# Performance work log

Measured on AMD Instinct MI355X. Metric: run time of the kernel, lower is better.

## Reference

```python
import jax, jax.numpy as jnp
import numpy as np

KNOW, ITEM, D, L, LAT, B, S = 1024, 20000, 128, 2, 256, 256, 200
NTOT = ITEM + KNOW
E1, E2 = 32768, 160000


def graph_layer(h, W, a, src, dst, n):
    # GAT-style: gather src/dst, edge MLP, segment softmax over dst, weighted scatter-sum
    z = h @ W                                              # [N, D]
    e = jax.nn.leaky_relu((jnp.concatenate([z[src], z[dst]], axis=-1) @ a)[:, 0])  # [E]
    m = jax.ops.segment_max(e, dst, num_segments=n)
    m = jnp.where(jnp.isfinite(m), m, 0.0)                 # nodes with no in-edges
    w = jnp.exp(e - m[dst])                                # [E]
    den = jax.ops.segment_sum(w, dst, num_segments=n)      # [N]
    num = jax.ops.segment_sum(w[:, None] * z[src], dst, num_segments=n)  # [N, D]
    return jnp.where(den[:, None] > 0, num / jnp.maximum(den, 1e-12)[:, None], 0.0)


def setup_inputs() -> dict:
    key = jax.random.key(0)
    ks = jax.random.split(key, 32)
    p = lambda i, shp: jax.random.normal(ks[i], shp, dtype=jnp.float32) * 0.05
    inp = {
        'p_rec': jax.random.randint(ks[0], (B, S), 0, ITEM),
        'p_target': jax.random.randint(ks[1], (B,), 0, S),
        'a_rec': jax.random.randint(ks[2], (B, S), 0, 3),
        'kn_rec': jax.random.uniform(ks[3], (B, S, KNOW), dtype=jnp.float32),
        'kn_num': jnp.ones((B, S), dtype=jnp.float32),
        'src1': jax.random.randint(ks[4], (E1,), 0, KNOW),
        'dst1': jax.random.randint(ks[5], (E1,), 0, KNOW),
        'src2': jax.random.randint(ks[6], (E2,), 0, NTOT),
        'dst2': jax.random.randint(ks[7], (E2,), 0, NTOT),
        'src3': jax.random.randint(ks[8], (E2,), 0, NTOT),
        'dst3': jax.random.randint(ks[9], (E2,), 0, NTOT),
        'kn_table': p(10, (KNOW, D)),
        'exer_table': p(11, (ITEM, D)),
        'ans_table': p(12, (3, D)),
        'gW': p(13, (L, 3, D, D)),
        'gA': p(14, (L, 3, 2 * D, 1)),
        'raW1': p(15, (L, D, D)),
        'raB1': jnp.zeros((L, D), jnp.float32),
        'raW2': p(16, (L, D, 1)),
        'actW1': p(17, (3 * D, LAT)),
        'actB1': jnp.zeros((LAT,), jnp.float32),
        'actW2': p(18, (LAT, ITEM)),
        'actB2': jnp.zeros((ITEM,), jnp.float32),
        'vW1': p(19, (3, 3 * D, LAT)),
        'vB1': jnp.zeros((3, LAT), jnp.float32),
        'vW2': p(20, (3, LAT, 1)),
        'vB2': jnp.zeros((3, 1), jnp.float32),
    }
    return inp


def reference(p_rec, p_target, a_rec, kn_rec, kn_num, src1, dst1, src2, dst2, src3, dst3,
              kn_table, exer_table, ans_table, gW, gA, raW1, raB1, raW2,
              actW1, actB1, actW2, actB2, vW1, vB1, vW2, vB2):
    kn, ex = kn_table, exer_table
    for l in range(L):  # GraphEncoder: stacked Fusion blocks (distinct params)
        k_dir = graph_layer(kn, gW[l, 0], gA[l, 0], src1, dst1, KNOW)
        ek = jnp.concatenate([ex, kn], axis=0)             # [NTOT, D]
        kfe = graph_layer(ek, gW[l, 1], gA[l, 1], src2, dst2, NTOT)
        efk = graph_layer(ek, gW[l, 2], gA[l, 2], src3, dst3, NTOT)
        A_, B_ = k_dir, kfe[ITEM:]
        ra = lambda x: jnp.tanh(x @ raW1[l] + raB1[l]) @ raW2[l]  # [KNOW, 1]
        s = jax.nn.softmax(jnp.concatenate([ra(A_), ra(B_)], axis=1), axis=1)
        kn = s[:, :1] * A_ + s[:, 1:2] * B_
        ex = efk[:ITEM]
    # hidden_layer
    be = ex[p_rec]                                         # [B, S, D]
    ba = ans_table[a_rec]                                  # [B, S, D]
    bk = jnp.einsum('bsk,kd->bsd', kn_rec, kn) / kn_num[..., None]
    item = jnp.concatenate([be, ba, bk], axis=-1)          # [B, S, 3D]
    m = (jnp.arange(S)[None, :] < (p_target + 1)[:, None]).astype(item.dtype)
    h = (item * m[..., None]).sum(axis=1) / m.sum(axis=1, keepdims=True)  # [B, 3D]
    logits = jnp.tanh(h @ actW1 + actB1) @ actW2 + actB2   # [B, ITEM]
    vh = jnp.tanh(jnp.einsum('bd,kdl->kbl', h, vW1) + vB1[:, None, :])
    vals = jnp.einsum('kbl,klo->kbo', vh, vW2) + vB2[:, None, :]  # [3, B, 1]
    return logits, vals[0], vals[1], vals[2]
```

## Files before the change

kernel.cpp:

```cpp
#include <hip/hip_runtime.h>

#define D 128
#define KNOW 1024
#define ITEM 20000
#define NTOT (ITEM + KNOW)
#define LAYERS 2
#define LAT 256
#define BB 256
#define SS 200
#define H3 (3 * D)
#define CH 8
#define ZROWS 64
#define NBK (KNOW / ZROWS)
#define NBN ((NTOT + ZROWS - 1) / ZROWS)
#define XPITCH 68

__global__ __launch_bounds__(256) void zdv(
    const float* __restrict__ Xe, const float* __restrict__ Xk,
    const float* __restrict__ gW, const float* __restrict__ gA, int layer,
    float* __restrict__ z1, float* __restrict__ z2, float* __restrict__ z3,
    float* __restrict__ ds1, float* __restrict__ dd1,
    float* __restrict__ ds2, float* __restrict__ dd2,
    float* __restrict__ ds3, float* __restrict__ dd3)
{
    __shared__ __align__(16) float xT[D * XPITCH];
    int bid = blockIdx.x;
    int g, row0, nmax;
    if (bid < NBK)            { g = 0; row0 = bid * ZROWS;                nmax = KNOW; }
    else if (bid < NBK + NBN) { g = 1; row0 = (bid - NBK) * ZROWS;        nmax = NTOT; }
    else                      { g = 2; row0 = (bid - NBK - NBN) * ZROWS;  nmax = NTOT; }
    const float* W = gW + (size_t)(layer * 3 + g) * D * D;
    const float* A = gA + (size_t)(layer * 3 + g) * 2 * D;
    float* Z  = (g == 0) ? z1  : (g == 1 ? z2  : z3);
    float* DS = (g == 0) ? ds1 : (g == 1 ? ds2 : ds3);
    float* DD = (g == 0) ? dd1 : (g == 1 ? dd2 : dd3);

    int tid = threadIdx.x;
#pragma unroll
    for (int i = 0; i < 8; ++i) {
        int flat = tid + i * 256;
        int row  = flat >> 5;
        int f4   = flat & 31;
        int grow = row0 + row;
        float4 v = make_float4(0.f, 0.f, 0.f, 0.f);
        if (grow < nmax) {
            const float* src = (g == 0) ? (Xk + (size_t)grow * D)
                             : (grow < ITEM ? Xe + (size_t)grow * D
                                            : Xk + (size_t)(grow - ITEM) * D);
            v = *(const float4*)(src + f4 * 4);
        }
        int slot = row ^ ((f4 & 7) << 2);
        int kk = f4 * 4;
        xT[(kk + 0) * XPITCH + slot] = v.x;
        xT[(kk + 1) * XPITCH + slot] = v.y;
        xT[(kk + 2) * XPITCH + slot] = v.z;
        xT[(kk + 3) * XPITCH + slot] = v.w;
    }
    __syncthreads();

    int cg = tid & 31;
    int rg = tid >> 5;
    int c0 = cg * 4;
    int r0a = rg * 8, r0b = rg * 8 + 4;

    float acc[8][4];
#pragma unroll
    for (int r = 0; r < 8; ++r)
#pragma unroll
        for (int c = 0; c < 4; ++c) acc[r][c] = 0.f;

#pragma unroll 4
    for (int k = 0; k < D; ++k) {
        float4 wv = *(const float4*)(W + (size_t)k * D + c0);
        int xc = ((k >> 2) & 7) << 2;
        float4 xa = *(const float4*)&xT[k * XPITCH + (r0a ^ xc)];
        float4 xb = *(const float4*)&xT[k * XPITCH + (r0b ^ xc)];
        acc[0][0] = fmaf(xa.x, wv.x, acc[0][0]); acc[0][1] = fmaf(xa.x, wv.y, acc[0][1]);
        acc[0][2] = fmaf(xa.x, wv.z, acc[0][2]); acc[0][3] = fmaf(xa.x, wv.w, acc[0][3]);
        acc[1][0] = fmaf(xa.y, wv.x, acc[1][0]); acc[1][1] = fmaf(xa.y, wv.y, acc[1][1]);
        acc[1][2] = fmaf(xa.y, wv.z, acc[1][2]); acc[1][3] = fmaf(xa.y, wv.w, acc[1][3]);
        acc[2][0] = fmaf(xa.z, wv.x, acc[2][0]); acc[2][1] = fmaf(xa.z, wv.y, acc[2][1]);
        acc[2][2] = fmaf(xa.z, wv.z, acc[2][2]); acc[2][3] = fmaf(xa.z, wv.w, acc[2][3]);
        acc[3][0] = fmaf(xa.w, wv.x, acc[3][0]); acc[3][1] = fmaf(xa.w, wv.y, acc[3][1]);
        acc[3][2] = fmaf(xa.w, wv.z, acc[3][2]); acc[3][3] = fmaf(xa.w, wv.w, acc[3][3]);
        acc[4][0] = fmaf(xb.x, wv.x, acc[4][0]); acc[4][1] = fmaf(xb.x, wv.y, acc[4][1]);
        acc[4][2] = fmaf(xb.x, wv.z, acc[4][2]); acc[4][3] = fmaf(xb.x, wv.w, acc[4][3]);
        acc[5][0] = fmaf(xb.y, wv.x, acc[5][0]); acc[5][1] = fmaf(xb.y, wv.y, acc[5][1]);
        acc[5][2] = fmaf(xb.y, wv.z, acc[5][2]); acc[5][3] = fmaf(xb.y, wv.w, acc[5][3]);
        acc[6][0] = fmaf(xb.z, wv.x, acc[6][0]); acc[6][1] = fmaf(xb.z, wv.y, acc[6][1]);
        acc[6][2] = fmaf(xb.z, wv.z, acc[6][2]); acc[6][3] = fmaf(xb.z, wv.w, acc[6][3]);
        acc[7][0] = fmaf(xb.w, wv.x, acc[7][0]); acc[7][1] = fmaf(xb.w, wv.y, acc[7][1]);
        acc[7][2] = fmaf(xb.w, wv.z, acc[7][2]); acc[7][3] = fmaf(xb.w, wv.w, acc[7][3]);
    }

#pragma unroll
    for (int r = 0; r < 8; ++r) {
        int grow = row0 + ((r < 4) ? (r0a + r) : (r0b + r - 4));
        if (grow < nmax) {
            float4 v = make_float4(acc[r][0], acc[r][1], acc[r][2], acc[r][3]);
            *(float4*)(Z + (size_t)grow * D + c0) = v;
        }
    }

    float4 as = *(const float4*)(A + c0);
    float4 ad = *(const float4*)(A + D + c0);
    float ps[8], pd[8];
#pragma unroll
    for (int r = 0; r < 8; ++r) {
        ps[r] = acc[r][0] * as.x + acc[r][1] * as.y + acc[r][2] * as.z + acc[r][3] * as.w;
        pd[r] = acc[r][0] * ad.x + acc[r][1] * ad.y + acc[r][2] * ad.z + acc[r][3] * ad.w;
    }
#pragma unroll
    for (int m = 16; m; m >>= 1) {
#pragma unroll
        for (int r = 0; r < 8; ++r) {
            ps[r] += __shfl_xor(ps[r], m, 64);
            pd[r] += __shfl_xor(pd[r], m, 64);
        }
    }
    if (cg == 0) {
#pragma unroll
        for (int r = 0; r < 8; ++r) {
            int grow = row0 + ((r < 4) ? (r0a + r) : (r0b + r - 4));
            if (grow < nmax) { DS[grow] = ps[r]; DD[grow] = pd[r]; }
        }
    }
}

__global__ void hist3(const int* __restrict__ d1, const int* __restrict__ d2, const int* __restrict__ d3,
                      int E1, int E2, int* __restrict__ c1, int* __restrict__ c2, int* __restrict__ c3) {
    int i = blockIdx.x * blockDim.x + threadIdx.x;
    if (i < E1) atomicAdd(&c1[d1[i]], 1);
    else if (i < E1 + E2) { int d = d2[i - E1]; if (d >= ITEM) atomicAdd(&c2[d - ITEM], 1); }
    else if (i < E1 + 2 * E2) { int d = d3[i - E1 - E2]; if (d < ITEM) atomicAdd(&c3[d], 1); }
}

__global__ __launch_bounds__(1024) void exscan3(int* __restrict__ c1, int* __restrict__ o1,
                                                int* __restrict__ c2, int* __restrict__ o2,
                                                int* __restrict__ c3, int* __restrict__ o3) {
    int g = blockIdx.x;
    int* cnt = (g == 0) ? c1 : (g == 1 ? c2 : c3);
    int* off = (g == 0) ? o1 : (g == 1 ? o2 : o3);
    int n = (g == 2) ? ITEM : KNOW;
    int tid = threadIdx.x, lane = tid & 63, wid = tid >> 6;
    int L = (n + 1023) >> 10;
    int i0 = tid * L;
    int sum = 0;
    for (int q = 0; q < L; ++q) {
        int i = i0 + q;
        if (i < n) sum += cnt[i];
    }
    int x = sum;
#pragma unroll
    for (int d = 1; d < 64; d <<= 1) { int t = __shfl_up(x, d, 64); if (lane >= d) x += t; }
    __shared__ int ws[16];
    if (lane == 63) ws[wid] = x;
    __syncthreads();
    if (wid == 0) {
        int w = (lane < 16) ? ws[lane] : 0;
#pragma unroll
        for (int d = 1; d < 16; d <<= 1) { int t = __shfl_up(w, d, 64); if (lane >= d) w += t; }
        if (lane < 16) ws[lane] = w;
    }
    __syncthreads();
    int run = x - sum + ((wid > 0) ? ws[wid - 1] : 0);
    if (tid == 0) off[0] = 0;
    for (int q = 0; q < L; ++q) {
        int i = i0 + q;
        if (i < n) {
            int v = cnt[i];
            cnt[i] = run;
            run += v;
            off[i + 1] = run;
        }
    }
}

__global__ void scatter3(const int* __restrict__ s1, const int* __restrict__ d1,
                         const int* __restrict__ s2, const int* __restrict__ d2,
                         const int* __restrict__ s3, const int* __restrict__ d3,
                         int E1, int E2, int* __restrict__ cur1, int* __restrict__ cur2, int* __restrict__ cur3,
                         int* __restrict__ e1, int* __restrict__ e2, int* __restrict__ e3) {
    int i = blockIdx.x * blockDim.x + threadIdx.x;
    if (i < E1) { int p = atomicAdd(&cur1[d1[i]], 1); e1[p] = s1[i]; }
    else if (i < E1 + E2) { int j = i - E1; int d = d2[j]; if (d >= ITEM) { int p = atomicAdd(&cur2[d - ITEM], 1); e2[p] = s2[j]; } }
    else if (i < E1 + 2 * E2) { int j = i - E1 - E2; int d = d3[j]; if (d < ITEM) { int p = atomicAdd(&cur3[d], 1); e3[p] = s3[j]; } }
}

__device__ __forceinline__ void agg_row(const float* __restrict__ Z, const float* __restrict__ dsrc,
                                        float dd, const int* __restrict__ es, int e0, int e1,
                                        int lane, float* __restrict__ acc) {
#pragma unroll
    for (int q = 0; q < 8; ++q) acc[q] = 0.f;
    if (e1 <= e0) return;
    float mx = -3.4e38f;
    for (int e = e0 + lane; e < e1; e += 64) {
        float t = dsrc[es[e]] + dd;
        t = (t > 0.f) ? t : 0.01f * t;
        mx = fmaxf(mx, t);
    }
#pragma unroll
    for (int o = 32; o; o >>= 1) mx = fmaxf(mx, __shfl_xor(mx, o, 64));
    int eg = lane >> 4, cs = lane & 15;
    float den = 0.f;
    for (int e = e0 + eg; e < e1; e += 4) {
        int s = es[e];
        float t = dsrc[s] + dd;
        t = (t > 0.f) ? t : 0.01f * t;
        float w = __expf(t - mx);
        den += w;
        const float4* zr = (const float4*)(Z + (size_t)s * D + cs * 8);
        float4 za = zr[0], zb = zr[1];
        acc[0] = fmaf(w, za.x, acc[0]); acc[1] = fmaf(w, za.y, acc[1]);
        acc[2] = fmaf(w, za.z, acc[2]); acc[3] = fmaf(w, za.w, acc[3]);
        acc[4] = fmaf(w, zb.x, acc[4]); acc[5] = fmaf(w, zb.y, acc[5]);
        acc[6] = fmaf(w, zb.z, acc[6]); acc[7] = fmaf(w, zb.w, acc[7]);
    }
#pragma unroll
    for (int m = 16; m <= 32; m <<= 1) {
        den += __shfl_xor(den, m, 64);
#pragma unroll
        for (int q = 0; q < 8; ++q) acc[q] += __shfl_xor(acc[q], m, 64);
    }
    float inv = 1.f / fmaxf(den, 1e-12f);
#pragma unroll
    for (int q = 0; q < 8; ++q) acc[q] *= inv;
}

__global__ __launch_bounds__(256) void agg3c(
    const float* __restrict__ z1, const float* __restrict__ z2, const float* __restrict__ z3,
    const float* __restrict__ ds1, const float* __restrict__ dd1,
    const float* __restrict__ ds2, const float* __restrict__ dd2,
    const float* __restrict__ ds3, const float* __restrict__ dd3,
    const int* __restrict__ off1, const int* __restrict__ es1,
    const int* __restrict__ off2, const int* __restrict__ es2,
    const int* __restrict__ off3, const int* __restrict__ es3,
    const float* __restrict__ raW1, const float* __restrict__ raB1,
    const float* __restrict__ raW2, float* __restrict__ buf)
{
    int wv = threadIdx.x >> 6, lane = threadIdx.x & 63;
    int eg = lane >> 4, cs = lane & 15;
    if (blockIdx.x < KNOW / 4) {
        __shared__ float ABs[4][2][D];
        int i = blockIdx.x * 4 + wv;
        float accA[8], accB[8];
        agg_row(z1, ds1, dd1[i], es1, off1[i], off1[i + 1], lane, accA);
        agg_row(z2, ds2, dd2[ITEM + i], es2, off2[i], off2[i + 1], lane, accB);
        if (eg == 0) {
            *(float4*)&ABs[wv][0][cs * 8]     = make_float4(accA[0], accA[1], accA[2], accA[3]);
            *(float4*)&ABs[wv][0][cs * 8 + 4] = make_float4(accA[4], accA[5], accA[6], accA[7]);
            *(float4*)&ABs[wv][1][cs * 8]     = make_float4(accB[0], accB[1], accB[2], accB[3]);
            *(float4*)&ABs[wv][1][cs * 8 + 4] = make_float4(accB[4], accB[5], accB[6], accB[7]);
        }
        __syncthreads();
        int j0 = lane * 2;
        float b0 = raB1[j0], b1 = raB1[j0 + 1];
        float aA0 = b0, aA1 = b1, aB0 = b0, aB1 = b1;
#pragma unroll 4
        for (int k = 0; k < D; ++k) {
            float av = ABs[wv][0][k], bv = ABs[wv][1][k];
            float2 w = *(const float2*)(raW1 + (size_t)k * D + j0);
            aA0 = fmaf(av, w.x, aA0); aA1 = fmaf(av, w.y, aA1);
            aB0 = fmaf(bv, w.x, aB0); aB1 = fmaf(bv, w.y, aB1);
        }
        float2 w2 = *(const float2*)(raW2 + j0);
        float pA = tanhf(aA0) * w2.x + tanhf(aA1) * w2.y;
        float pB = tanhf(aB0) * w2.x + tanhf(aB1) * w2.y;
#pragma unroll
        for (int o = 32; o; o >>= 1) { pA += __shfl_xor(pA, o, 64); pB += __shfl_xor(pB, o, 64); }
        float mx2 = fmaxf(pA, pB);
        float eA = __expf(pA - mx2), eB = __expf(pB - mx2);
        float s = 1.f / (eA + eB);
        float sA = eA * s, sB = eB * s;
        float2 Av = *(float2*)&ABs[wv][0][j0];
        float2 Bv = *(float2*)&ABs[wv][1][j0];
        *(float2*)(buf + (size_t)(ITEM + i) * D + j0) =
            make_float2(sA * Av.x + sB * Bv.x, sA * Av.y + sB * Bv.y);
    } else {
        int row = (blockIdx.x - KNOW / 4) * 4 + wv;
        if (row < ITEM) {
            float acc[8];
            agg_row(z3, ds3, dd3[row], es3, off3[row], off3[row + 1], lane, acc);
            if (eg == 0) {
                *(float4*)(buf + (size_t)row * D + cs * 8)     = make_float4(acc[0], acc[1], acc[2], acc[3]);
                *(float4*)(buf + (size_t)row * D + cs * 8 + 4) = make_float4(acc[4], acc[5], acc[6], acc[7]);
            }
        }
    }
}

__global__ __launch_bounds__(256) void krowk(const float* __restrict__ kn_rec, const float* __restrict__ kn_num,
                                             const int* __restrict__ p_target, float* __restrict__ krowP) {
    int b = blockIdx.x, ch = blockIdx.y;
    int cnt = p_target[b] + 1;
    int per = (SS + CH - 1) / CH;
    int s0 = ch * per, s1 = s0 + per;
    if (s1 > cnt) s1 = cnt;
    int k0 = threadIdx.x * 4;
    float4 a = make_float4(0.f, 0.f, 0.f, 0.f);
    for (int s = s0; s < s1; ++s) {
        float inv = 1.f / kn_num[b * SS + s];
        float4 v = *(const float4*)(kn_rec + ((size_t)b * SS + s) * KNOW + k0);
        a.x += v.x * inv; a.y += v.y * inv; a.z += v.z * inv; a.w += v.w * inv;
    }
    *(float4*)(krowP + ((size_t)ch * BB + b) * KNOW + k0) = a;
}

__global__ __launch_bounds__(512) void hker(const float* __restrict__ ex, const float* __restrict__ ans_table,
                                            const int* __restrict__ p_rec, const int* __restrict__ a_rec,
                                            const int* __restrict__ p_target, const float* __restrict__ krowP,
                                            const float* __restrict__ kn, float* __restrict__ h) {
    int b = blockIdx.x;
    int j = threadIdx.x & 127, sg = threadIdx.x >> 7;
    int cnt = p_target[b] + 1;
    __shared__ int pidx[SS], aidx[SS];
    __shared__ float kr[KNOW];
    __shared__ float red[4][3][128];
    for (int i = threadIdx.x; i < cnt; i += 512) { pidx[i] = p_rec[b * SS + i]; aidx[i] = a_rec[b * SS + i]; }
    for (int i = threadIdx.x; i < KNOW; i += 512) {
        float s = 0.f;
#pragma unroll
        for (int c = 0; c < CH; ++c) s += krowP[((size_t)c * BB + b) * KNOW + i];
        kr[i] = s;
    }
    __syncthreads();
    float accE = 0.f, accA = 0.f;
    for (int s = sg; s < cnt; s += 4) {
        accE += ex[(size_t)pidx[s] * D + j];
        accA += ans_table[aidx[s] * D + j];
    }
    float accK = 0.f;
    for (int k = sg * 256; k < sg * 256 + 256; ++k) accK += kr[k] * kn[(size_t)k * D + j];
    red[sg][0][j] = accE; red[sg][1][j] = accA; red[sg][2][j] = accK;
    __syncthreads();
    if (sg == 0) {
        float inv = 1.f / (float)cnt;
        float e = (red[0][0][j] + red[1][0][j] + red[2][0][j] + red[3][0][j]) * inv;
        float a = (red[0][1][j] + red[1][1][j] + red[2][1][j] + red[3][1][j]) * inv;
        float kv = (red[0][2][j] + red[1][2][j] + red[2][2][j] + red[3][2][j]) * inv;
        h[b * H3 + j] = e;
        h[b * H3 + D + j] = a;
        h[b * H3 + 2 * D + j] = kv;
    }
}

__global__ __launch_bounds__(256) void hidden_gemm(const float* __restrict__ h,
                                                   const float* __restrict__ actW1, const float* __restrict__ actB1,
                                                   const float* __restrict__ vW1, const float* __restrict__ vB1,
                                                   float* __restrict__ hid) {
    __shared__ float hT[H3 * 17];
    int tid = threadIdx.x;
    int b0 = blockIdx.y * 16;
    for (int idx = tid; idx < 16 * H3; idx += 256) {
        int r = idx / H3, k = idx - r * H3;
        hT[k * 17 + r] = h[(size_t)(b0 + r) * H3 + k];
    }
    __syncthreads();
    int j = blockIdx.x * 64 + (tid & 63);
    int head = j >> 8, jj = j & 255;
    int rg = tid >> 6, r0 = rg * 4;
    const float* W = (head == 0) ? actW1 : (vW1 + (size_t)(head - 1) * H3 * LAT);
    float bias = (head == 0) ? actB1[jj] : vB1[(head - 1) * LAT + jj];
    float acc[4] = {bias, bias, bias, bias};
#pragma unroll 4
    for (int k = 0; k < H3; ++k) {
        float w = W[(size_t)k * LAT + jj];
        float h0 = hT[k * 17 + r0 + 0];
        float h1 = hT[k * 17 + r0 + 1];
        float h2 = hT[k * 17 + r0 + 2];
        float h3 = hT[k * 17 + r0 + 3];
        acc[0] = fmaf(h0, w, acc[0]);
        acc[1] = fmaf(h1, w, acc[1]);
        acc[2] = fmaf(h2, w, acc[2]);
        acc[3] = fmaf(h3, w, acc[3]);
    }
#pragma unroll
    for (int r = 0; r < 4; ++r)
        hid[((size_t)head * BB + (b0 + r0 + r)) * LAT + jj] = tanhf(acc[r]);
}

__global__ __launch_bounds__(256) void logitsker(const float* __restrict__ hid, const float* __restrict__ actW2,
                                                 const float* __restrict__ actB2, float* __restrict__ out) {
    __shared__ float hT[LAT * 33];
    int tid = threadIdx.x;
    int b0 = blockIdx.y * 32;
    for (int idx = tid; idx < 32 * LAT; idx += 256) {
        int r = idx >> 8, k = idx & 255;
        hT[k * 33 + r] = hid[(size_t)(b0 + r) * LAT + k];
    }
    __syncthreads();
    int lane6 = tid & 63;
    int rg = tid >> 6, r0 = rg * 8;
    int ibase = blockIdx.x * 256 + lane6;
    int icol[4], icl[4];
    float bias[4];
#pragma unroll
    for (int c = 0; c < 4; ++c) {
        icol[c] = ibase + c * 64;
        icl[c] = icol[c] < ITEM ? icol[c] : (ITEM - 1);
        bias[c] = actB2[icl[c]];
    }
    float acc[8][4];
#pragma unroll
    for (int r = 0; r < 8; ++r)
#pragma unroll
        for (int c = 0; c < 4; ++c) acc[r][c] = bias[c];
#pragma unroll 2
    for (int k = 0; k < LAT; ++k) {
        float w0 = actW2[(size_t)k * ITEM + icl[0]];
        float w1 = actW2[(size_t)k * ITEM + icl[1]];
        float w2 = actW2[(size_t)k * ITEM + icl[2]];
        float w3 = actW2[(size_t)k * ITEM + icl[3]];
        const float* hp = &hT[k * 33 + r0];
#pragma unroll
        for (int r = 0; r < 8; ++r) {
            float hv = hp[r];
            acc[r][0] = fmaf(hv, w0, acc[r][0]);
            acc[r][1] = fmaf(hv, w1, acc[r][1]);
            acc[r][2] = fmaf(hv, w2, acc[r][2]);
            acc[r][3] = fmaf(hv, w3, acc[r][3]);
        }
    }
#pragma unroll
    for (int c = 0; c < 4; ++c) {
        if (icol[c] < ITEM) {
#pragma unroll
            for (int r = 0; r < 8; ++r)
                out[(size_t)(b0 + r0 + r) * ITEM + icol[c]] = acc[r][c];
        }
    }
}

__global__ __launch_bounds__(256) void valsker(const float* __restrict__ hid, const float* __restrict__ vW2,
                                               const float* __restrict__ vB2, float* __restrict__ out) {
    int idx = blockIdx.x * 4 + (threadIdx.x >> 6);
    int lane = threadIdx.x & 63;
    if (idx >= 3 * BB) return;
    int k = idx / BB, b = idx - k * BB;
    const float* vh = hid + ((size_t)(k + 1) * BB + b) * LAT;
    float4 a = ((const float4*)vh)[lane];
    float4 w = ((const float4*)(vW2 + k * LAT))[lane];
    float s = a.x * w.x + a.y * w.y + a.z * w.z + a.w * w.w;
#pragma unroll
    for (int o = 32; o; o >>= 1) s += __shfl_down(s, o, 64);
    if (lane == 0) out[(size_t)BB * ITEM + k * BB + b] = s + vB2[k];
}

extern "C" void kernel_launch(void* const* d_in, const int* in_sizes, int n_in,
                              void* d_out, int out_size, void* d_ws, size_t ws_size,
                              hipStream_t stream) {
    const int*   p_rec      = (const int*)d_in[0];
    const int*   p_target   = (const int*)d_in[1];
    const int*   a_rec      = (const int*)d_in[2];
    const float* kn_rec     = (const float*)d_in[3];
    const float* kn_num     = (const float*)d_in[4];
    const int*   src1       = (const int*)d_in[5];
    const int*   dst1       = (const int*)d_in[6];
    const int*   src2       = (const int*)d_in[7];
    const int*   dst2       = (const int*)d_in[8];
    const int*   src3       = (const int*)d_in[9];
    const int*   dst3       = (const int*)d_in[10];
    const float* kn_table   = (const float*)d_in[11];
    const float* exer_table = (const float*)d_in[12];
    const float* ans_table  = (const float*)d_in[13];
    const float* gW         = (const float*)d_in[14];
    const float* gA         = (const float*)d_in[15];
    const float* raW1       = (const float*)d_in[16];
    const float* raB1       = (const float*)d_in[17];
    const float* raW2       = (const float*)d_in[18];
    const float* actW1      = (const float*)d_in[19];
    const float* actB1      = (const float*)d_in[20];
    const float* actW2      = (const float*)d_in[21];
    const float* actB2      = (const float*)d_in[22];
    const float* vW1        = (const float*)d_in[23];
    const float* vB1        = (const float*)d_in[24];
    const float* vW2        = (const float*)d_in[25];
    const float* vB2        = (const float*)d_in[26];
    const int E1 = in_sizes[5], E2 = in_sizes[7];

    float* base = (float*)d_ws;
    size_t o = 0;
    auto alloc = [&](size_t n) -> float* { float* p = base + o; o += (n + 3) & ~(size_t)3; return p; };
    float* buf  = alloc((size_t)NTOT * D);
    float* z1   = alloc((size_t)KNOW * D);
    float* z2   = alloc((size_t)NTOT * D);
    float* z3   = alloc((size_t)NTOT * D);
    float* ds1 = alloc(KNOW);  float* dd1 = alloc(KNOW);
    float* ds2 = alloc(NTOT);  float* dd2 = alloc(NTOT);
    float* ds3 = alloc(NTOT);  float* dd3 = alloc(NTOT);
    int* cnts = (int*)alloc(2 * KNOW + NTOT);
    int* cnt1 = cnts, *cnt2 = cnts + KNOW, *cnt3 = cnts + 2 * KNOW;
    int* off1 = (int*)alloc(KNOW + 1);
    int* off2 = (int*)alloc(KNOW + 1);
    int* off3 = (int*)alloc(ITEM + 1);
    int* es1  = (int*)alloc(E1);
    int* es2  = (int*)alloc(E2);
    int* es3  = (int*)alloc(E2);
    float* krowP = alloc((size_t)CH * BB * KNOW);
    float* hbuf  = alloc((size_t)BB * H3);
    float* hid   = alloc((size_t)4 * BB * LAT);

    hipMemsetAsync(cnts, 0, sizeof(int) * (2 * KNOW + NTOT), stream);

    int etot = E1 + 2 * E2;
    hist3<<<(etot + 255) / 256, 256, 0, stream>>>(dst1, dst2, dst3, E1, E2, cnt1, cnt2, cnt3);
    exscan3<<<3, 1024, 0, stream>>>(cnt1, off1, cnt2, off2, cnt3, off3);
    scatter3<<<(etot + 255) / 256, 256, 0, stream>>>(src1, dst1, src2, dst2, src3, dst3,
                                                     E1, E2, cnt1, cnt2, cnt3, es1, es2, es3);

    int aggBlocks = KNOW / 4 + ITEM / 4;
    for (int l = 0; l < LAYERS; ++l) {
        const float* Xe = (l == 0) ? exer_table : buf;
        const float* Xk = (l == 0) ? kn_table : (buf + (size_t)ITEM * D);
        zdv<<<NBK + 2 * NBN, 256, 0, stream>>>(Xe, Xk, gW, gA, l, z1, z2, z3,
                                               ds1, dd1, ds2, dd2, ds3, dd3);
        agg3c<<<aggBlocks, 256, 0, stream>>>(z1, z2, z3, ds1, dd1, ds2, dd2, ds3, dd3,
                                             off1, es1, off2, es2, off3, es3,
                                             raW1 + (size_t)l * D * D, raB1 + (size_t)l * D,
                                             raW2 + (size_t)l * D, buf);
    }

    krowk<<<dim3(BB, CH), 256, 0, stream>>>(kn_rec, kn_num, p_target, krowP);
    hker<<<BB, 512, 0, stream>>>(buf, ans_table, p_rec, a_rec, p_target, krowP, buf + (size_t)ITEM * D, hbuf);
    hidden_gemm<<<dim3(16, 16), 256, 0, stream>>>(hbuf, actW1, actB1, vW1, vB1, hid);
    logitsker<<<dim3((ITEM + 255) / 256, 8), 256, 0, stream>>>(hid, actW2, actB2, (float*)d_out);
    valsker<<<(3 * BB + 3) / 4, 256, 0, stream>>>(hid, vW2, vB2, (float*)d_out);
}
```

Before: 312.7 us.

## Fuse graph layers and krow reduction into a persistent cooperative kernel

```diff
diff --git a/kernel.cpp b/kernel.cpp
--- a/kernel.cpp
+++ b/kernel.cpp
@@ -1,4 +1,7 @@
 #include <hip/hip_runtime.h>
+#include <hip/hip_cooperative_groups.h>
+
+namespace cg = cooperative_groups;
 
 #define D 128
 #define KNOW 1024
@@ -13,18 +16,20 @@
 #define ZROWS 64
 #define NBK (KNOW / ZROWS)
 #define NBN ((NTOT + ZROWS - 1) / ZROWS)
+#define NZT (NBK + 2 * NBN)
+#define NAGGU (KNOW / 4 + ITEM / 4)
+#define NKROW (BB * CH)
 #define XPITCH 68
-
-__global__ __launch_bounds__(256) void zdv(
+#define MGRID 256
+
+__device__ __forceinline__ void zdv_tile(int bid, int layer, float* __restrict__ xT,
     const float* __restrict__ Xe, const float* __restrict__ Xk,
-    const float* __restrict__ gW, const float* __restrict__ gA, int layer,
+    const float* __restrict__ gW, const float* __restrict__ gA,
     float* __restrict__ z1, float* __restrict__ z2, float* __restrict__ z3,
     float* __restrict__ ds1, float* __restrict__ dd1,
     float* __restrict__ ds2, float* __restrict__ dd2,
     float* __restrict__ ds3, float* __restrict__ dd3)
 {
-    __shared__ __align__(16) float xT[D * XPITCH];
-    int bid = blockIdx.x;
     int g, row0, nmax;
     if (bid < NBK)            { g = 0; row0 = bid * ZROWS;                nmax = KNOW; }
     else if (bid < NBK + NBN) { g = 1; row0 = (bid - NBK) * ZROWS;        nmax = NTOT; }
@@ -36,6 +41,7 @@
     float* DD = (g == 0) ? dd1 : (g == 1 ? dd2 : dd3);
 
     int tid = threadIdx.x;
+    __syncthreads();
 #pragma unroll
     for (int i = 0; i < 8; ++i) {
         int flat = tid + i * 256;
@@ -58,9 +64,9 @@
     }
     __syncthreads();
 
-    int cg = tid & 31;
+    int cg_ = tid & 31;
     int rg = tid >> 5;
-    int c0 = cg * 4;
+    int c0 = cg_ * 4;
     int r0a = rg * 8, r0b = rg * 8 + 4;
 
     float acc[8][4];
@@ -118,73 +124,13 @@
             pd[r] += __shfl_xor(pd[r], m, 64);
         }
     }
-    if (cg == 0) {
+    if (cg_ == 0) {
 #pragma unroll
         for (int r = 0; r < 8; ++r) {
             int grow = row0 + ((r < 4) ? (r0a + r) : (r0b + r - 4));
             if (grow < nmax) { DS[grow] = ps[r]; DD[grow] = pd[r]; }
         }
     }
-}
-
-__global__ void hist3(const int* __restrict__ d1, const int* __restrict__ d2, const int* __restrict__ d3,
-                      int E1, int E2, int* __restrict__ c1, int* __restrict__ c2, int* __restrict__ c3) {
-    int i = blockIdx.x * blockDim.x + threadIdx.x;
-    if (i < E1) atomicAdd(&c1[d1[i]], 1);
-    else if (i < E1 + E2) { int d = d2[i - E1]; if (d >= ITEM) atomicAdd(&c2[d - ITEM], 1); }
-    else if (i < E1 + 2 * E2) { int d = d3[i - E1 - E2]; if (d < ITEM) atomicAdd(&c3[d], 1); }
-}
-
-__global__ __launch_bounds__(1024) void exscan3(int* __restrict__ c1, int* __restrict__ o1,
-                                                int* __restrict__ c2, int* __restrict__ o2,
-                                                int* __restrict__ c3, int* __restrict__ o3) {
-    int g = blockIdx.x;
-    int* cnt = (g == 0) ? c1 : (g == 1 ? c2 : c3);
-    int* off = (g == 0) ? o1 : (g == 1 ? o2 : o3);
-    int n = (g == 2) ? ITEM : KNOW;
-    int tid = threadIdx.x, lane = tid & 63, wid = tid >> 6;
-    int L = (n + 1023) >> 10;
-    int i0 = tid * L;
-    int sum = 0;
-    for (int q = 0; q < L; ++q) {
-        int i = i0 + q;
-        if (i < n) sum += cnt[i];
-    }
-    int x = sum;
-#pragma unroll
-    for (int d = 1; d < 64; d <<= 1) { int t = __shfl_up(x, d, 64); if (lane >= d) x += t; }
-    __shared__ int ws[16];
-    if (lane == 63) ws[wid] = x;
-    __syncthreads();
-    if (wid == 0) {
-        int w = (lane < 16) ? ws[lane] : 0;
-#pragma unroll
-        for (int d = 1; d < 16; d <<= 1) { int t = __shfl_up(w, d, 64); if (lane >= d) w += t; }
-        if (lane < 16) ws[lane] = w;
-    }
-    __syncthreads();
-    int run = x - sum + ((wid > 0) ? ws[wid - 1] : 0);
-    if (tid == 0) off[0] = 0;
-    for (int q = 0; q < L; ++q) {
-        int i = i0 + q;
-        if (i < n) {
-            int v = cnt[i];
-            cnt[i] = run;
-            run += v;
-            off[i + 1] = run;
-        }
-    }
-}
-
-__global__ void scatter3(const int* __restrict__ s1, const int* __restrict__ d1,
-                         const int* __restrict__ s2, const int* __restrict__ d2,
-                         const int* __restrict__ s3, const int* __restrict__ d3,
-                         int E1, int E2, int* __restrict__ cur1, int* __restrict__ cur2, int* __restrict__ cur3,
-                         int* __restrict__ e1, int* __restrict__ e2, int* __restrict__ e3) {
-    int i = blockIdx.x * blockDim.x + threadIdx.x;
-    if (i < E1) { int p = atomicAdd(&cur1[d1[i]], 1); e1[p] = s1[i]; }
-    else if (i < E1 + E2) { int j = i - E1; int d = d2[j]; if (d >= ITEM) { int p = atomicAdd(&cur2[d - ITEM], 1); e2[p] = s2[j]; } }
-    else if (i < E1 + 2 * E2) { int j = i - E1 - E2; int d = d3[j]; if (d < ITEM) { int p = atomicAdd(&cur3[d], 1); e3[p] = s3[j]; } }
 }
 
 __device__ __forceinline__ void agg_row(const float* __restrict__ Z, const float* __restrict__ dsrc,
@@ -227,7 +173,7 @@
     for (int q = 0; q < 8; ++q) acc[q] *= inv;
 }
 
-__global__ __launch_bounds__(256) void agg3c(
+__device__ __forceinline__ void agg_unit(int u, float (*ABs)[2][D],
     const float* __restrict__ z1, const float* __restrict__ z2, const float* __restrict__ z3,
     const float* __restrict__ ds1, const float* __restrict__ dd1,
     const float* __restrict__ ds2, const float* __restrict__ dd2,
@@ -235,14 +181,14 @@
     const int* __restrict__ off1, const int* __restrict__ es1,
     const int* __restrict__ off2, const int* __restrict__ es2,
     const int* __restrict__ off3, const int* __restrict__ es3,
-    const float* __restrict__ raW1, const float* __restrict__ raB1,
-    const float* __restrict__ raW2, float* __restrict__ buf)
+    const float* __restrict__ raW1L, const float* __restrict__ raB1L,
+    const float* __restrict__ raW2L, float* __restrict__ buf)
 {
     int wv = threadIdx.x >> 6, lane = threadIdx.x & 63;
     int eg = lane >> 4, cs = lane & 15;
-    if (blockIdx.x < KNOW / 4) {
-        __shared__ float ABs[4][2][D];
-        int i = blockIdx.x * 4 + wv;
+    if (u < KNOW / 4) {
+        __syncthreads();
+        int i = u * 4 + wv;
         float accA[8], accB[8];
         agg_row(z1, ds1, dd1[i], es1, off1[i], off1[i + 1], lane, accA);
         agg_row(z2, ds2, dd2[ITEM + i], es2, off2[i], off2[i + 1], lane, accB);
@@ -254,16 +200,16 @@
         }
         __syncthreads();
         int j0 = lane * 2;
-        float b0 = raB1[j0], b1 = raB1[j0 + 1];
+        float b0 = raB1L[j0], b1 = raB1L[j0 + 1];
         float aA0 = b0, aA1 = b1, aB0 = b0, aB1 = b1;
 #pragma unroll 4
         for (int k = 0; k < D; ++k) {
             float av = ABs[wv][0][k], bv = ABs[wv][1][k];
-            float2 w = *(const float2*)(raW1 + (size_t)k * D + j0);
+            float2 w = *(const float2*)(raW1L + (size_t)k * D + j0);
             aA0 = fmaf(av, w.x, aA0); aA1 = fmaf(av, w.y, aA1);
             aB0 = fmaf(bv, w.x, aB0); aB1 = fmaf(bv, w.y, aB1);
         }
-        float2 w2 = *(const float2*)(raW2 + j0);
+        float2 w2 = *(const float2*)(raW2L + j0);
         float pA = tanhf(aA0) * w2.x + tanhf(aA1) * w2.y;
         float pB = tanhf(aB0) * w2.x + tanhf(aB1) * w2.y;
 #pragma unroll
@@ -277,7 +223,7 @@
         *(float2*)(buf + (size_t)(ITEM + i) * D + j0) =
             make_float2(sA * Av.x + sB * Bv.x, sA * Av.y + sB * Bv.y);
     } else {
-        int row = (blockIdx.x - KNOW / 4) * 4 + wv;
+        int row = (u - KNOW / 4) * 4 + wv;
         if (row < ITEM) {
             float acc[8];
             agg_row(z3, ds3, dd3[row], es3, off3[row], off3[row + 1], lane, acc);
@@ -289,9 +235,11 @@
     }
 }
 
-__global__ __launch_bounds__(256) void krowk(const float* __restrict__ kn_rec, const float* __restrict__ kn_num,
-                                             const int* __restrict__ p_target, float* __restrict__ krowP) {
-    int b = blockIdx.x, ch = blockIdx.y;
+__device__ __forceinline__ void krow_unit(int uk, const float* __restrict__ kn_rec,
+                                          const float* __restrict__ kn_num,
+                                          const int* __restrict__ p_target, float* __restrict__ krowP)
+{
+    int b = uk & (BB - 1), ch = uk >> 8;
     int cnt = p_target[b] + 1;
     int per = (SS + CH - 1) / CH;
     int s0 = ch * per, s1 = s0 + per;
@@ -304,6 +252,132 @@
         a.x += v.x * inv; a.y += v.y * inv; a.z += v.z * inv; a.w += v.w * inv;
     }
     *(float4*)(krowP + ((size_t)ch * BB + b) * KNOW + k0) = a;
+}
+
+__global__ __launch_bounds__(256) void megaker(
+    const float* Xe0, const float* Xk0, const float* gW, const float* gA,
+    float* buf, float* z1, float* z2, float* z3,
+    float* ds1, float* dd1, float* ds2, float* dd2, float* ds3, float* dd3,
+    const int* off1, const int* es1, const int* off2, const int* es2,
+    const int* off3, const int* es3,
+    const float* raW1, const float* raB1, const float* raW2,
+    const float* kn_rec, const float* kn_num, const int* p_target, float* krowP)
+{
+    cg::grid_group grid = cg::this_grid();
+    __shared__ __align__(16) float xT[D * XPITCH];
+    __shared__ float ABs[4][2][D];
+    for (int l = 0; l < LAYERS; ++l) {
+        const float* Xe = (l == 0) ? Xe0 : buf;
+        const float* Xk = (l == 0) ? Xk0 : (buf + (size_t)ITEM * D);
+        for (int t = blockIdx.x; t < NZT; t += MGRID)
+            zdv_tile(t, l, xT, Xe, Xk, gW, gA, z1, z2, z3, ds1, dd1, ds2, dd2, ds3, dd3);
+        grid.sync();
+        int nu = NAGGU + ((l == 0) ? NKROW : 0);
+        for (int u = blockIdx.x; u < nu; u += MGRID) {
+            if (u < NAGGU)
+                agg_unit(u, ABs, z1, z2, z3, ds1, dd1, ds2, dd2, ds3, dd3,
+                         off1, es1, off2, es2, off3, es3,
+                         raW1 + (size_t)l * D * D, raB1 + (size_t)l * D, raW2 + (size_t)l * D, buf);
+            else
+                krow_unit(u - NAGGU, kn_rec, kn_num, p_target, krowP);
+        }
+        grid.sync();
+    }
+}
+
+__global__ __launch_bounds__(256) void zdv_ker(
+    const float* __restrict__ Xe, const float* __restrict__ Xk,
+    const float* __restrict__ gW, const float* __restrict__ gA, int layer,
+    float* __restrict__ z1, float* __restrict__ z2, float* __restrict__ z3,
+    float* __restrict__ ds1, float* __restrict__ dd1,
+    float* __restrict__ ds2, float* __restrict__ dd2,
+    float* __restrict__ ds3, float* __restrict__ dd3)
+{
+    __shared__ __align__(16) float xT[D * XPITCH];
+    zdv_tile(blockIdx.x, layer, xT, Xe, Xk, gW, gA, z1, z2, z3, ds1, dd1, ds2, dd2, ds3, dd3);
+}
+
+__global__ __launch_bounds__(256) void agg3c_ker(
+    const float* __restrict__ z1, const float* __restrict__ z2, const float* __restrict__ z3,
+    const float* __restrict__ ds1, const float* __restrict__ dd1,
+    const float* __restrict__ ds2, const float* __restrict__ dd2,
+    const float* __restrict__ ds3, const float* __restrict__ dd3,
+    const int* __restrict__ off1, const int* __restrict__ es1,
+    const int* __restrict__ off2, const int* __restrict__ es2,
+    const int* __restrict__ off3, const int* __restrict__ es3,
+    const float* __restrict__ raW1L, const float* __restrict__ raB1L,
+    const float* __restrict__ raW2L, float* __restrict__ buf)
+{
+    __shared__ float ABs[4][2][D];
+    agg_unit(blockIdx.x, ABs, z1, z2, z3, ds1, dd1, ds2, dd2, ds3, dd3,
+             off1, es1, off2, es2, off3, es3, raW1L, raB1L, raW2L, buf);
+}
+
+__global__ __launch_bounds__(256) void krowk_ker(const float* __restrict__ kn_rec,
+                                                 const float* __restrict__ kn_num,
+                                                 const int* __restrict__ p_target,
+                                                 float* __restrict__ krowP) {
+    krow_unit(blockIdx.y * BB + blockIdx.x, kn_rec, kn_num, p_target, krowP);
+}
+
+__global__ void hist3(const int* __restrict__ d1, const int* __restrict__ d2, const int* __restrict__ d3,
+                      int E1, int E2, int* __restrict__ c1, int* __restrict__ c2, int* __restrict__ c3) {
+    int i = blockIdx.x * blockDim.x + threadIdx.x;
+    if (i < E1) atomicAdd(&c1[d1[i]], 1);
+    else if (i < E1 + E2) { int d = d2[i - E1]; if (d >= ITEM) atomicAdd(&c2[d - ITEM], 1); }
+    else if (i < E1 + 2 * E2) { int d = d3[i - E1 - E2]; if (d < ITEM) atomicAdd(&c3[d], 1); }
+}
+
+__global__ __launch_bounds__(1024) void exscan3(int* __restrict__ c1, int* __restrict__ o1,
+                                                int* __restrict__ c2, int* __restrict__ o2,
+                                                int* __restrict__ c3, int* __restrict__ o3) {
+    int g = blockIdx.x;
+    int* cnt = (g == 0) ? c1 : (g == 1 ? c2 : c3);
+    int* off = (g == 0) ? o1 : (g == 1 ? o2 : o3);
+    int n = (g == 2) ? ITEM : KNOW;
+    int tid = threadIdx.x, lane = tid & 63, wid = tid >> 6;
+    int L = (n + 1023) >> 10;
+    int i0 = tid * L;
+    int sum = 0;
+    for (int q = 0; q < L; ++q) {
+        int i = i0 + q;
+        if (i < n) sum += cnt[i];
+    }
+    int x = sum;
+#pragma unroll
+    for (int d = 1; d < 64; d <<= 1) { int t = __shfl_up(x, d, 64); if (lane >= d) x += t; }
+    __shared__ int ws[16];
+    if (lane == 63) ws[wid] = x;
+    __syncthreads();
+    if (wid == 0) {
+        int w = (lane < 16) ? ws[lane] : 0;
+#pragma unroll
+        for (int d = 1; d < 16; d <<= 1) { int t = __shfl_up(w, d, 64); if (lane >= d) w += t; }
+        if (lane < 16) ws[lane] = w;
+    }
+    __syncthreads();
+    int run = x - sum + ((wid > 0) ? ws[wid - 1] : 0);
+    if (tid == 0) off[0] = 0;
+    for (int q = 0; q < L; ++q) {
+        int i = i0 + q;
+        if (i < n) {
+            int v = cnt[i];
+            cnt[i] = run;
+            run += v;
+            off[i + 1] = run;
+        }
+    }
+}
+
+__global__ void scatter3(const int* __restrict__ s1, const int* __restrict__ d1,
+                         const int* __restrict__ s2, const int* __restrict__ d2,
+                         const int* __restrict__ s3, const int* __restrict__ d3,
+                         int E1, int E2, int* __restrict__ cur1, int* __restrict__ cur2, int* __restrict__ cur3,
+                         int* __restrict__ e1, int* __restrict__ e2, int* __restrict__ e3) {
+    int i = blockIdx.x * blockDim.x + threadIdx.x;
+    if (i < E1) { int p = atomicAdd(&cur1[d1[i]], 1); e1[p] = s1[i]; }
+    else if (i < E1 + E2) { int j = i - E1; int d = d2[j]; if (d >= ITEM) { int p = atomicAdd(&cur2[d - ITEM], 1); e2[p] = s2[j]; } }
+    else if (i < E1 + 2 * E2) { int j = i - E1 - E2; int d = d3[j]; if (d < ITEM) { int p = atomicAdd(&cur3[d], 1); e3[p] = s3[j]; } }
 }
 
 __global__ __launch_bounds__(512) void hker(const float* __restrict__ ex, const float* __restrict__ ans_table,
@@ -508,19 +582,31 @@
     scatter3<<<(etot + 255) / 256, 256, 0, stream>>>(src1, dst1, src2, dst2, src3, dst3,
                                                      E1, E2, cnt1, cnt2, cnt3, es1, es2, es3);
 
-    int aggBlocks = KNOW / 4 + ITEM / 4;
-    for (int l = 0; l < LAYERS; ++l) {
-        const float* Xe = (l == 0) ? exer_table : buf;
-        const float* Xk = (l == 0) ? kn_table : (buf + (size_t)ITEM * D);
-        zdv<<<NBK + 2 * NBN, 256, 0, stream>>>(Xe, Xk, gW, gA, l, z1, z2, z3,
-                                               ds1, dd1, ds2, dd2, ds3, dd3);
-        agg3c<<<aggBlocks, 256, 0, stream>>>(z1, z2, z3, ds1, dd1, ds2, dd2, ds3, dd3,
-                                             off1, es1, off2, es2, off3, es3,
-                                             raW1 + (size_t)l * D * D, raB1 + (size_t)l * D,
-                                             raW2 + (size_t)l * D, buf);
-    }
-
-    krowk<<<dim3(BB, CH), 256, 0, stream>>>(kn_rec, kn_num, p_target, krowP);
+    const float* Xe0 = exer_table;
+    const float* Xk0 = kn_table;
+    void* args[] = {
+        (void*)&Xe0, (void*)&Xk0, (void*)&gW, (void*)&gA,
+        (void*)&buf, (void*)&z1, (void*)&z2, (void*)&z3,
+        (void*)&ds1, (void*)&dd1, (void*)&ds2, (void*)&dd2, (void*)&ds3, (void*)&dd3,
+        (void*)&off1, (void*)&es1, (void*)&off2, (void*)&es2, (void*)&off3, (void*)&es3,
+        (void*)&raW1, (void*)&raB1, (void*)&raW2,
+        (void*)&kn_rec, (void*)&kn_num, (void*)&p_target, (void*)&krowP
+    };
+    hipError_t ce = hipLaunchCooperativeKernel((void*)megaker, dim3(MGRID), dim3(256), args, 0, stream);
+    if (ce != hipSuccess) {
+        for (int l = 0; l < LAYERS; ++l) {
+            const float* Xe = (l == 0) ? exer_table : buf;
+            const float* Xk = (l == 0) ? kn_table : (buf + (size_t)ITEM * D);
+            zdv_ker<<<NZT, 256, 0, stream>>>(Xe, Xk, gW, gA, l, z1, z2, z3,
+                                             ds1, dd1, ds2, dd2, ds3, dd3);
+            agg3c_ker<<<NAGGU, 256, 0, stream>>>(z1, z2, z3, ds1, dd1, ds2, dd2, ds3, dd3,
+                                                 off1, es1, off2, es2, off3, es3,
+                                                 raW1 + (size_t)l * D * D, raB1 + (size_t)l * D,
+                                                 raW2 + (size_t)l * D, buf);
+        }
+        krowk_ker<<<dim3(BB, CH), 256, 0, stream>>>(kn_rec, kn_num, p_target, krowP);
+    }
+
     hker<<<BB, 512, 0, stream>>>(buf, ans_table, p_rec, a_rec, p_target, krowP, buf + (size_t)ITEM * D, hbuf);
     hidden_gemm<<<dim3(16, 16), 256, 0, stream>>>(hbuf, actW1, actB1, vW1, vB1, hid);
     logitsker<<<dim3((ITEM + 255) / 256, 8), 256, 0, stream>>>(hid, actW2, actB2, (float*)d_out);
```

Result: slower. 697.6 us, median of 2 (+123.1%).

## Fuse krowk into layer-0 aggregation and merge logits with value heads

Applied to the files above, without the earlier changes.

```diff
diff --git a/kernel.cpp b/kernel.cpp
--- a/kernel.cpp
+++ b/kernel.cpp
@@ -9,13 +9,19 @@
 #define BB 256
 #define SS 200
 #define H3 (3 * D)
-#define CH 8
+#define CH 4
 #define ZROWS 64
 #define NBK (KNOW / ZROWS)
 #define NBN ((NTOT + ZROWS - 1) / ZROWS)
+#define NZT (NBK + 2 * NBN)
+#define NAGGU (KNOW / 4 + ITEM / 4)
+#define NKROW (BB * CH)
 #define XPITCH 68
-
-__global__ __launch_bounds__(256) void zdv(
+#define NLOGB ((ITEM + 255) / 256)
+#define NLV (NLOGB * (BB / 32))
+#define NVB ((3 * BB + 3) / 4)
+
+__global__ __launch_bounds__(256) void zdv_ker(
     const float* __restrict__ Xe, const float* __restrict__ Xk,
     const float* __restrict__ gW, const float* __restrict__ gA, int layer,
     float* __restrict__ z1, float* __restrict__ z2, float* __restrict__ z3,
@@ -58,9 +64,9 @@
     }
     __syncthreads();
 
-    int cg = tid & 31;
+    int cg_ = tid & 31;
     int rg = tid >> 5;
-    int c0 = cg * 4;
+    int c0 = cg_ * 4;
     int r0a = rg * 8, r0b = rg * 8 + 4;
 
     float acc[8][4];
@@ -118,7 +124,7 @@
             pd[r] += __shfl_xor(pd[r], m, 64);
         }
     }
-    if (cg == 0) {
+    if (cg_ == 0) {
 #pragma unroll
         for (int r = 0; r < 8; ++r) {
             int grow = row0 + ((r < 4) ? (r0a + r) : (r0b + r - 4));
@@ -235,14 +241,17 @@
     const int* __restrict__ off1, const int* __restrict__ es1,
     const int* __restrict__ off2, const int* __restrict__ es2,
     const int* __restrict__ off3, const int* __restrict__ es3,
-    const float* __restrict__ raW1, const float* __restrict__ raB1,
-    const float* __restrict__ raW2, float* __restrict__ buf)
+    const float* __restrict__ raW1L, const float* __restrict__ raB1L,
+    const float* __restrict__ raW2L, float* __restrict__ buf,
+    const float* __restrict__ kn_rec, const float* __restrict__ kn_num,
+    const int* __restrict__ p_target, float* __restrict__ krowP)
 {
     int wv = threadIdx.x >> 6, lane = threadIdx.x & 63;
     int eg = lane >> 4, cs = lane & 15;
-    if (blockIdx.x < KNOW / 4) {
+    int u = blockIdx.x;
+    if (u < KNOW / 4) {
         __shared__ float ABs[4][2][D];
-        int i = blockIdx.x * 4 + wv;
+        int i = u * 4 + wv;
         float accA[8], accB[8];
         agg_row(z1, ds1, dd1[i], es1, off1[i], off1[i + 1], lane, accA);
         agg_row(z2, ds2, dd2[ITEM + i], es2, off2[i], off2[i + 1], lane, accB);
@@ -254,16 +263,16 @@
         }
         __syncthreads();
         int j0 = lane * 2;
-        float b0 = raB1[j0], b1 = raB1[j0 + 1];
+        float b0 = raB1L[j0], b1 = raB1L[j0 + 1];
         float aA0 = b0, aA1 = b1, aB0 = b0, aB1 = b1;
 #pragma unroll 4
         for (int k = 0; k < D; ++k) {
             float av = ABs[wv][0][k], bv = ABs[wv][1][k];
-            float2 w = *(const float2*)(raW1 + (size_t)k * D + j0);
+            float2 w = *(const float2*)(raW1L + (size_t)k * D + j0);
             aA0 = fmaf(av, w.x, aA0); aA1 = fmaf(av, w.y, aA1);
             aB0 = fmaf(bv, w.x, aB0); aB1 = fmaf(bv, w.y, aB1);
         }
-        float2 w2 = *(const float2*)(raW2 + j0);
+        float2 w2 = *(const float2*)(raW2L + j0);
         float pA = tanhf(aA0) * w2.x + tanhf(aA1) * w2.y;
         float pB = tanhf(aB0) * w2.x + tanhf(aB1) * w2.y;
 #pragma unroll
@@ -276,8 +285,8 @@
         float2 Bv = *(float2*)&ABs[wv][1][j0];
         *(float2*)(buf + (size_t)(ITEM + i) * D + j0) =
             make_float2(sA * Av.x + sB * Bv.x, sA * Av.y + sB * Bv.y);
-    } else {
-        int row = (blockIdx.x - KNOW / 4) * 4 + wv;
+    } else if (u < NAGGU) {
+        int row = (u - KNOW / 4) * 4 + wv;
         if (row < ITEM) {
             float acc[8];
             agg_row(z3, ds3, dd3[row], es3, off3[row], off3[row + 1], lane, acc);
@@ -286,24 +295,22 @@
                 *(float4*)(buf + (size_t)row * D + cs * 8 + 4) = make_float4(acc[4], acc[5], acc[6], acc[7]);
             }
         }
-    }
-}
-
-__global__ __launch_bounds__(256) void krowk(const float* __restrict__ kn_rec, const float* __restrict__ kn_num,
-                                             const int* __restrict__ p_target, float* __restrict__ krowP) {
-    int b = blockIdx.x, ch = blockIdx.y;
-    int cnt = p_target[b] + 1;
-    int per = (SS + CH - 1) / CH;
-    int s0 = ch * per, s1 = s0 + per;
-    if (s1 > cnt) s1 = cnt;
-    int k0 = threadIdx.x * 4;
-    float4 a = make_float4(0.f, 0.f, 0.f, 0.f);
-    for (int s = s0; s < s1; ++s) {
-        float inv = 1.f / kn_num[b * SS + s];
-        float4 v = *(const float4*)(kn_rec + ((size_t)b * SS + s) * KNOW + k0);
-        a.x += v.x * inv; a.y += v.y * inv; a.z += v.z * inv; a.w += v.w * inv;
-    }
-    *(float4*)(krowP + ((size_t)ch * BB + b) * KNOW + k0) = a;
+    } else {
+        int uk = u - NAGGU;
+        int b = uk & (BB - 1), ch = uk >> 8;
+        int cnt = p_target[b] + 1;
+        int per = (SS + CH - 1) / CH;
+        int s0 = ch * per, s1 = s0 + per;
+        if (s1 > cnt) s1 = cnt;
+        int k0 = threadIdx.x * 4;
+        float4 a = make_float4(0.f, 0.f, 0.f, 0.f);
+        for (int s = s0; s < s1; ++s) {
+            float inv = 1.f / kn_num[b * SS + s];
+            float4 v = *(const float4*)(kn_rec + ((size_t)b * SS + s) * KNOW + k0);
+            a.x += v.x * inv; a.y += v.y * inv; a.z += v.z * inv; a.w += v.w * inv;
+        }
+        *(float4*)(krowP + ((size_t)ch * BB + b) * KNOW + k0) = a;
+    }
 }
 
 __global__ __launch_bounds__(512) void hker(const float* __restrict__ ex, const float* __restrict__ ans_table,
@@ -379,71 +386,74 @@
         hid[((size_t)head * BB + (b0 + r0 + r)) * LAT + jj] = tanhf(acc[r]);
 }
 
-__global__ __launch_bounds__(256) void logitsker(const float* __restrict__ hid, const float* __restrict__ actW2,
-                                                 const float* __restrict__ actB2, float* __restrict__ out) {
-    __shared__ float hT[LAT * 33];
+__global__ __launch_bounds__(256) void logitsvals(const float* __restrict__ hid,
+                                                  const float* __restrict__ actW2, const float* __restrict__ actB2,
+                                                  const float* __restrict__ vW2, const float* __restrict__ vB2,
+                                                  float* __restrict__ out) {
+    int bid = blockIdx.x;
     int tid = threadIdx.x;
-    int b0 = blockIdx.y * 32;
-    for (int idx = tid; idx < 32 * LAT; idx += 256) {
-        int r = idx >> 8, k = idx & 255;
-        hT[k * 33 + r] = hid[(size_t)(b0 + r) * LAT + k];
-    }
-    __syncthreads();
-    int lane6 = tid & 63;
-    int rg = tid >> 6, r0 = rg * 8;
-    int ibase = blockIdx.x * 256 + lane6;
-    int icol[4], icl[4];
-    float bias[4];
-#pragma unroll
-    for (int c = 0; c < 4; ++c) {
-        icol[c] = ibase + c * 64;
-        icl[c] = icol[c] < ITEM ? icol[c] : (ITEM - 1);
-        bias[c] = actB2[icl[c]];
-    }
-    float acc[8][4];
-#pragma unroll
-    for (int r = 0; r < 8; ++r)
-#pragma unroll
-        for (int c = 0; c < 4; ++c) acc[r][c] = bias[c];
+    if (bid < NLV) {
+        __shared__ float hT[LAT * 33];
+        int ix = bid % NLOGB, iy = bid / NLOGB;
+        int b0 = iy * 32;
+        for (int idx = tid; idx < 32 * LAT; idx += 256) {
+            int r = idx >> 8, k = idx & 255;
+            hT[k * 33 + r] = hid[(size_t)(b0 + r) * LAT + k];
+        }
+        __syncthreads();
+        int lane6 = tid & 63;
+        int rg = tid >> 6, r0 = rg * 8;
+        int ibase = ix * 256 + lane6;
+        int icol[4], icl[4];
+        float bias[4];
+#pragma unroll
+        for (int c = 0; c < 4; ++c) {
+            icol[c] = ibase + c * 64;
+            icl[c] = icol[c] < ITEM ? icol[c] : (ITEM - 1);
+            bias[c] = actB2[icl[c]];
+        }
+        float acc[8][4];
+#pragma unroll
+        for (int r = 0; r < 8; ++r)
+#pragma unroll
+            for (int c = 0; c < 4; ++c) acc[r][c] = bias[c];
 #pragma unroll 2
-    for (int k = 0; k < LAT; ++k) {
-        float w0 = actW2[(size_t)k * ITEM + icl[0]];
-        float w1 = actW2[(size_t)k * ITEM + icl[1]];
-        float w2 = actW2[(size_t)k * ITEM + icl[2]];
-        float w3 = actW2[(size_t)k * ITEM + icl[3]];
-        const float* hp = &hT[k * 33 + r0];
-#pragma unroll
-        for (int r = 0; r < 8; ++r) {
-            float hv = hp[r];
-            acc[r][0] = fmaf(hv, w0, acc[r][0]);
-            acc[r][1] = fmaf(hv, w1, acc[r][1]);
-            acc[r][2] = fmaf(hv, w2, acc[r][2]);
-            acc[r][3] = fmaf(hv, w3, acc[r][3]);
-        }
-    }
-#pragma unroll
-    for (int c = 0; c < 4; ++c) {
-        if (icol[c] < ITEM) {
-#pragma unroll
-            for (int r = 0; r < 8; ++r)
-                out[(size_t)(b0 + r0 + r) * ITEM + icol[c]] = acc[r][c];
-        }
-    }
-}
-
-__global__ __launch_bounds__(256) void valsker(const float* __restrict__ hid, const float* __restrict__ vW2,
-                                               const float* __restrict__ vB2, float* __restrict__ out) {
-    int idx = blockIdx.x * 4 + (threadIdx.x >> 6);
-    int lane = threadIdx.x & 63;
-    if (idx >= 3 * BB) return;
-    int k = idx / BB, b = idx - k * BB;
-    const float* vh = hid + ((size_t)(k + 1) * BB + b) * LAT;
-    float4 a = ((const float4*)vh)[lane];
-    float4 w = ((const float4*)(vW2 + k * LAT))[lane];
-    float s = a.x * w.x + a.y * w.y + a.z * w.z + a.w * w.w;
-#pragma unroll
-    for (int o = 32; o; o >>= 1) s += __shfl_down(s, o, 64);
-    if (lane == 0) out[(size_t)BB * ITEM + k * BB + b] = s + vB2[k];
+        for (int k = 0; k < LAT; ++k) {
+            float w0 = actW2[(size_t)k * ITEM + icl[0]];
+            float w1 = actW2[(size_t)k * ITEM + icl[1]];
+            float w2 = actW2[(size_t)k * ITEM + icl[2]];
+            float w3 = actW2[(size_t)k * ITEM + icl[3]];
+            const float* hp = &hT[k * 33 + r0];
+#pragma unroll
+            for (int r = 0; r < 8; ++r) {
+                float hv = hp[r];
+                acc[r][0] = fmaf(hv, w0, acc[r][0]);
+                acc[r][1] = fmaf(hv, w1, acc[r][1]);
+                acc[r][2] = fmaf(hv, w2, acc[r][2]);
+                acc[r][3] = fmaf(hv, w3, acc[r][3]);
+            }
+        }
+#pragma unroll
+        for (int c = 0; c < 4; ++c) {
+            if (icol[c] < ITEM) {
+#pragma unroll
+                for (int r = 0; r < 8; ++r)
+                    out[(size_t)(b0 + r0 + r) * ITEM + icol[c]] = acc[r][c];
+            }
+        }
+    } else {
+        int idx = (bid - NLV) * 4 + (tid >> 6);
+        int lane = tid & 63;
+        if (idx >= 3 * BB) return;
+        int k = idx / BB, b = idx - k * BB;
+        const float* vh = hid + ((size_t)(k + 1) * BB + b) * LAT;
+        float4 a = ((const float4*)vh)[lane];
+        float4 w = ((const float4*)(vW2 + k * LAT))[lane];
+        float s = a.x * w.x + a.y * w.y + a.z * w.z + a.w * w.w;
+#pragma unroll
+        for (int o = 32; o; o >>= 1) s += __shfl_down(s, o, 64);
+        if (lane == 0) out[(size_t)BB * ITEM + k * BB + b] = s + vB2[k];
+    }
 }
 
 extern "C" void kernel_launch(void* const* d_in, const int* in_sizes, int n_in,
@@ -508,21 +518,20 @@
     scatter3<<<(etot + 255) / 256, 256, 0, stream>>>(src1, dst1, src2, dst2, src3, dst3,
                                                      E1, E2, cnt1, cnt2, cnt3, es1, es2, es3);
 
-    int aggBlocks = KNOW / 4 + ITEM / 4;
     for (int l = 0; l < LAYERS; ++l) {
         const float* Xe = (l == 0) ? exer_table : buf;
         const float* Xk = (l == 0) ? kn_table : (buf + (size_t)ITEM * D);
-        zdv<<<NBK + 2 * NBN, 256, 0, stream>>>(Xe, Xk, gW, gA, l, z1, z2, z3,
-                                               ds1, dd1, ds2, dd2, ds3, dd3);
-        agg3c<<<aggBlocks, 256, 0, stream>>>(z1, z2, z3, ds1, dd1, ds2, dd2, ds3, dd3,
-                                             off1, es1, off2, es2, off3, es3,
-                                             raW1 + (size_t)l * D * D, raB1 + (size_t)l * D,
-                                             raW2 + (size_t)l * D, buf);
-    }
-
-    krowk<<<dim3(BB, CH), 256, 0, stream>>>(kn_rec, kn_num, p_target, krowP);
+        zdv_ker<<<NZT, 256, 0, stream>>>(Xe, Xk, gW, gA, l, z1, z2, z3,
+                                         ds1, dd1, ds2, dd2, ds3, dd3);
+        int nb = NAGGU + ((l == 0) ? NKROW : 0);
+        agg3c<<<nb, 256, 0, stream>>>(z1, z2, z3, ds1, dd1, ds2, dd2, ds3, dd3,
+                                      off1, es1, off2, es2, off3, es3,
+                                      raW1 + (size_t)l * D * D, raB1 + (size_t)l * D,
+                                      raW2 + (size_t)l * D, buf,
+                                      kn_rec, kn_num, p_target, krowP);
+    }
+
     hker<<<BB, 512, 0, stream>>>(buf, ans_table, p_rec, a_rec, p_target, krowP, buf + (size_t)ITEM * D, hbuf);
     hidden_gemm<<<dim3(16, 16), 256, 0, stream>>>(hbuf, actW1, actB1, vW1, vB1, hid);
-    logitsker<<<dim3((ITEM + 255) / 256, 8), 256, 0, stream>>>(hid, actW2, actB2, (float*)d_out);
-    valsker<<<(3 * BB + 3) / 4, 256, 0, stream>>>(hid, vW2, vB2, (float*)d_out);
-}
+    logitsvals<<<NLV + NVB, 256, 0, stream>>>(hid, actW2, actB2, vW2, vB2, (float*)d_out);
+}
```

Result: faster. 303.5 us (-2.9%).
